# Optimization experiments

Hardware: AMD Instinct MI355X
Metric: run time of the kernel (lower is better)

## Reference

```python
import jax, jax.numpy as jnp
import numpy as np

F = 26          # number of sparse fields
V = 100000      # vocab per field
D = 32          # embedding dim
DENSE = 13
HID = (1024, 512, 256)
B = 16384


def setup_inputs() -> dict:
    key = jax.random.key(0)
    ks = jax.random.split(key, 16)
    x_sparse = jax.random.randint(ks[0], (B, F), 0, V, dtype=jnp.int32)
    x_dense = jax.random.normal(ks[1], (B, DENSE), dtype=jnp.float32)
    emb_tables = jax.random.normal(ks[2], (F, V, D), dtype=jnp.float32) * 0.05
    lin_tables = jax.random.normal(ks[3], (F, V), dtype=jnp.float32) * 0.05
    dnn_in = F * D + DENSE
    dims = (dnn_in,) + HID
    params = {}
    for i in range(len(HID)):
        params[f'W{i}'] = jax.random.normal(ks[4 + i], (dims[i], dims[i + 1]), dtype=jnp.float32) * (1.0 / np.sqrt(dims[i]))
        params[f'b{i}'] = jnp.zeros((dims[i + 1],), dtype=jnp.float32)
    Wout = jax.random.normal(ks[10], (HID[-1], 1), dtype=jnp.float32) * (1.0 / np.sqrt(HID[-1]))
    bout = jnp.zeros((1,), dtype=jnp.float32)
    return dict(x_sparse=x_sparse, x_dense=x_dense, emb_tables=emb_tables,
                lin_tables=lin_tables,
                W0=params['W0'], b0=params['b0'],
                W1=params['W1'], b1=params['b1'],
                W2=params['W2'], b2=params['b2'],
                Wout=Wout, bout=bout)


def reference(x_sparse, x_dense, emb_tables, lin_tables,
              W0, b0, W1, b1, W2, b2, Wout, bout):
    f_idx = jnp.arange(F)[None, :]            # [1, F]
    # batched multi-field gather: [B, F, D] and [B, F]
    emb = emb_tables[f_idx, x_sparse]          # [B, F, D]
    lin = lin_tables[f_idx, x_sparse]          # [B, F]
    linear_logit = lin.sum(axis=1)             # [B]
    # FM pairwise sum_{i<j} <e_i, e_j> via sum-square identity
    s = emb.sum(axis=1)                        # [B, D]
    fm_logit = 0.5 * ((s * s).sum(axis=-1) - (emb * emb).sum(axis=(1, 2)))  # [B]
    # DNN on concatenated embeddings + dense feats
    h = jnp.concatenate([emb.reshape(emb.shape[0], F * D), x_dense], axis=1)
    h = jax.nn.relu(h @ W0 + b0)
    h = jax.nn.relu(h @ W1 + b1)
    h = jax.nn.relu(h @ W2 + b2)
    dnn_logit = (h @ Wout + bout)[:, 0]        # [B]
    return jax.nn.sigmoid(linear_logit + fm_logit + dnn_logit)
```

## Files before the change

### kernel.cpp

```cpp
#include <hip/hip_runtime.h>
#include <math.h>


typedef __attribute__((ext_vector_type(8))) short shortx8;
typedef __attribute__((ext_vector_type(4))) float floatx4;

#define AS1 __attribute__((address_space(1)))
#define AS3 __attribute__((address_space(3)))

__device__ __forceinline__ void load_lds_16(const void* g, void* l) {
    __builtin_amdgcn_global_load_lds((AS1 void*)g, (AS3 void*)l, 16, 0, 0);
}

__device__ __forceinline__ unsigned short f2bf(float x) {
    union { float f; unsigned int u; } v; v.f = x;
    unsigned int r = v.u + 0x7fffu + ((v.u >> 16) & 1u);
    return (unsigned short)(r >> 16);
}

__global__ void wtrans(const float* __restrict__ W, unsigned short* __restrict__ Wt,
                       int K, int N, int Kpad)
{
    __shared__ float tile[32][33];
    const int k0 = blockIdx.x * 32, n0 = blockIdx.y * 32;
    const int tx = threadIdx.x, ty = threadIdx.y;
#pragma unroll
    for (int i = 0; i < 32; i += 8) {
        int k = k0 + ty + i;
        tile[ty + i][tx] = (k < K) ? W[(size_t)k * N + (n0 + tx)] : 0.f;
    }
    __syncthreads();
#pragma unroll
    for (int i = 0; i < 32; i += 8) {
        int n = n0 + ty + i, kk = k0 + tx;
        Wt[(size_t)n * Kpad + kk] = f2bf(tile[tx][ty + i]);
    }
}

__global__ __launch_bounds__(256)
void gather_fm(const int* __restrict__ xs, const float* __restrict__ xd,
               const float* __restrict__ emb, const float* __restrict__ lint,
               unsigned short* __restrict__ h0, float* __restrict__ lg)
{
    const int lane = threadIdx.x & 63;
    const int wave = threadIdx.x >> 6;
    const int b = blockIdx.x * 4 + wave;

    int idx = 0; float linv = 0.f;
    if (lane < 26) {
        idx = xs[b * 26 + lane];
        linv = lint[(size_t)lane * 100000 + idx];
    }
    const int d = lane & 31;
    const int half = lane >> 5;
    float s = 0.f, sq = 0.f;
    unsigned short* hrow = h0 + (size_t)b * 864;
#pragma unroll
    for (int it = 0; it < 13; ++it) {
        int f = it * 2 + half;
        int fidx = __shfl(idx, f);
        float v = emb[((size_t)f * 100000 + (size_t)fidx) * 32 + d];
        s += v; sq += v * v;
        hrow[f * 32 + d] = f2bf(v);
    }
    s += __shfl_xor(s, 32);
    float t = 0.25f * s * s - 0.5f * sq + linv;
#pragma unroll
    for (int off = 32; off >= 1; off >>= 1) t += __shfl_xor(t, off);
    if (lane == 0) lg[b] = t;

    if (lane < 13) {
        hrow[832 + lane] = f2bf(xd[b * 13 + lane]);
    } else if (lane < 32) {
        hrow[832 + lane] = 0;
    }
}

__global__ __launch_bounds__(256, 2)
void gemm_bign(const unsigned short* __restrict__ X,
               const unsigned short* __restrict__ Wt,
               const float* __restrict__ bias,
               unsigned short* __restrict__ Y,
               int M, int N, int K)
{
    __shared__ alignas(16) unsigned short As[128 * 32];
    __shared__ alignas(16) unsigned short Bs[256 * 32];

    const int tid  = threadIdx.x;
    const int lane = tid & 63;
    const int wave = tid >> 6;
    const int bm = blockIdx.x * 128;
    const int bn = blockIdx.y * 256;
    const int wm = (wave & 1) * 64;
    const int wn = (wave >> 1) * 128;
    const int lrow  = lane & 15;
    const int lquad = lane >> 4;

    floatx4 acc[4][8];
    const floatx4 z4 = {0.f, 0.f, 0.f, 0.f};
#pragma unroll
    for (int i = 0; i < 4; ++i)
#pragma unroll
        for (int j = 0; j < 8; ++j) acc[i][j] = z4;

    const int ar = tid >> 2, akp = (tid & 3) << 3;

    for (int k0 = 0; k0 < K; k0 += 32) {
        load_lds_16(X + (size_t)(bm + ar) * K + (k0 + akp), As + (size_t)tid * 8);
        load_lds_16(X + (size_t)(bm + ar + 64) * K + (k0 + akp), As + (size_t)(tid + 256) * 8);
#pragma unroll
        for (int q = 0; q < 4; ++q) {
            int c = tid + q * 256;
            load_lds_16(Wt + (size_t)(bn + (c >> 2)) * K + (k0 + akp), Bs + (size_t)c * 8);
        }
        __syncthreads();

        shortx8 a[4];
#pragma unroll
        for (int i = 0; i < 4; ++i)
            a[i] = *(const shortx8*)(As + (wm + i * 16 + lrow) * 32 + lquad * 8);
#pragma unroll
        for (int j = 0; j < 8; ++j) {
            shortx8 b = *(const shortx8*)(Bs + (wn + j * 16 + lrow) * 32 + lquad * 8);
#pragma unroll
            for (int i = 0; i < 4; ++i)
                acc[i][j] = __builtin_amdgcn_mfma_f32_16x16x32_bf16(a[i], b, acc[i][j], 0, 0, 0);
        }
        __syncthreads();
    }

#pragma unroll
    for (int i = 0; i < 4; ++i) {
        const int row = bm + wm + i * 16 + lquad * 4;
#pragma unroll
        for (int j = 0; j < 8; ++j) {
            const int col = bn + wn + j * 16 + lrow;
            const float bv = bias[col];
#pragma unroll
            for (int r = 0; r < 4; ++r) {
                float v = fmaxf(acc[i][j][r] + bv, 0.f);
                Y[(size_t)(row + r) * N + col] = f2bf(v);
            }
        }
    }
}

__global__ __launch_bounds__(256)
void gemm_bias_relu(const unsigned short* __restrict__ X,
                    const unsigned short* __restrict__ Wt,
                    const float* __restrict__ bias,
                    unsigned short* __restrict__ Y,
                    int M, int N, int K)
{
    __shared__ alignas(16) unsigned short As[128 * 32];
    __shared__ alignas(16) unsigned short Bs[128 * 32];

    const int tid  = threadIdx.x;
    const int lane = tid & 63;
    const int wave = tid >> 6;
    const int bm = blockIdx.x * 128;
    const int bn = blockIdx.y * 128;
    const int wm = (wave & 1) * 64;
    const int wn = (wave >> 1) * 64;
    const int lrow  = lane & 15;
    const int lquad = lane >> 4;

    floatx4 acc[4][4];
    const floatx4 z4 = {0.f, 0.f, 0.f, 0.f};
#pragma unroll
    for (int i = 0; i < 4; ++i)
#pragma unroll
        for (int j = 0; j < 4; ++j) acc[i][j] = z4;

    const int r0 = tid >> 2, kp0 = (tid & 3) << 3;

    for (int k0 = 0; k0 < K; k0 += 32) {
        load_lds_16(X  + (size_t)(bm + r0) * K + (k0 + kp0), As + (size_t)tid * 8);
        load_lds_16(Wt + (size_t)(bn + r0) * K + (k0 + kp0), Bs + (size_t)tid * 8);
        load_lds_16(X  + (size_t)(bm + r0 + 64) * K + (k0 + kp0), As + (size_t)(tid + 256) * 8);
        load_lds_16(Wt + (size_t)(bn + r0 + 64) * K + (k0 + kp0), Bs + (size_t)(tid + 256) * 8);
        __syncthreads();

        shortx8 a[4], b[4];
#pragma unroll
        for (int i = 0; i < 4; ++i)
            a[i] = *(const shortx8*)(As + (wm + i * 16 + lrow) * 32 + lquad * 8);
#pragma unroll
        for (int j = 0; j < 4; ++j)
            b[j] = *(const shortx8*)(Bs + (wn + j * 16 + lrow) * 32 + lquad * 8);
#pragma unroll
        for (int i = 0; i < 4; ++i)
#pragma unroll
            for (int j = 0; j < 4; ++j)
                acc[i][j] = __builtin_amdgcn_mfma_f32_16x16x32_bf16(a[i], b[j], acc[i][j], 0, 0, 0);
        __syncthreads();
    }

#pragma unroll
    for (int i = 0; i < 4; ++i) {
        const int row = bm + wm + i * 16 + lquad * 4;
#pragma unroll
        for (int j = 0; j < 4; ++j) {
            const int col = bn + wn + j * 16 + lrow;
            const float bv = bias[col];
#pragma unroll
            for (int r = 0; r < 4; ++r) {
                float v = fmaxf(acc[i][j][r] + bv, 0.f);
                Y[(size_t)(row + r) * N + col] = f2bf(v);
            }
        }
    }
}

__global__ __launch_bounds__(256)
void gemm3_final(const unsigned short* __restrict__ X,
                 const unsigned short* __restrict__ Wt,
                 const float* __restrict__ bias,
                 const float* __restrict__ Wo,
                 const float* __restrict__ bo,
                 const float* __restrict__ lg,
                 float* __restrict__ out)
{
    const int K = 512;
    __shared__ alignas(16) unsigned short As[64 * 32];
    __shared__ alignas(16) unsigned short Bs[256 * 32];
    __shared__ float red[4][64];

    const int tid  = threadIdx.x;
    const int lane = tid & 63;
    const int wave = tid >> 6;
    const int bm = blockIdx.x * 64;
    const int wn = wave * 64;
    const int lrow  = lane & 15;
    const int lquad = lane >> 4;

    floatx4 acc[4][4];
    const floatx4 z4 = {0.f, 0.f, 0.f, 0.f};
#pragma unroll
    for (int i = 0; i < 4; ++i)
#pragma unroll
        for (int j = 0; j < 4; ++j) acc[i][j] = z4;

    const int ar = tid >> 2, akp = (tid & 3) << 3;

    for (int k0 = 0; k0 < K; k0 += 32) {
        load_lds_16(X + (size_t)(bm + ar) * K + (k0 + akp), As + (size_t)tid * 8);
#pragma unroll
        for (int q = 0; q < 4; ++q) {
            int c = tid + q * 256;
            load_lds_16(Wt + (size_t)(c >> 2) * K + (k0 + akp), Bs + (size_t)c * 8);
        }
        __syncthreads();

        shortx8 a[4], b[4];
#pragma unroll
        for (int i = 0; i < 4; ++i)
            a[i] = *(const shortx8*)(As + (i * 16 + lrow) * 32 + lquad * 8);
#pragma unroll
        for (int j = 0; j < 4; ++j)
            b[j] = *(const shortx8*)(Bs + (wn + j * 16 + lrow) * 32 + lquad * 8);
#pragma unroll
        for (int i = 0; i < 4; ++i)
#pragma unroll
            for (int j = 0; j < 4; ++j)
                acc[i][j] = __builtin_amdgcn_mfma_f32_16x16x32_bf16(a[i], b[j], acc[i][j], 0, 0, 0);
        __syncthreads();
    }

    float bv[4], wv[4];
#pragma unroll
    for (int j = 0; j < 4; ++j) {
        int col = wn + j * 16 + lrow;
        bv[j] = bias[col];
        wv[j] = Wo[col];
    }
#pragma unroll
    for (int i = 0; i < 4; ++i) {
#pragma unroll
        for (int r = 0; r < 4; ++r) {
            float p = 0.f;
#pragma unroll
            for (int j = 0; j < 4; ++j) {
                float v = fmaxf(acc[i][j][r] + bv[j], 0.f);
                p += v * wv[j];
            }
            p += __shfl_xor(p, 1);
            p += __shfl_xor(p, 2);
            p += __shfl_xor(p, 4);
            p += __shfl_xor(p, 8);
            if (lrow == 0) red[wave][i * 16 + lquad * 4 + r] = p;
        }
    }
    __syncthreads();
    if (tid < 64) {
        float s = red[0][tid] + red[1][tid] + red[2][tid] + red[3][tid];
        float x = s + bo[0] + lg[bm + tid];
        out[bm + tid] = 1.f / (1.f + expf(-x));
    }
}

extern "C" void kernel_launch(void* const* d_in, const int* in_sizes, int n_in,
                              void* d_out, int out_size, void* d_ws, size_t ws_size,
                              hipStream_t stream)
{
    const int*   xs = (const int*)d_in[0];
    const float* xd = (const float*)d_in[1];
    const float* em = (const float*)d_in[2];
    const float* li = (const float*)d_in[3];
    const float* W0 = (const float*)d_in[4];
    const float* b0 = (const float*)d_in[5];
    const float* W1 = (const float*)d_in[6];
    const float* b1 = (const float*)d_in[7];
    const float* W2 = (const float*)d_in[8];
    const float* b2 = (const float*)d_in[9];
    const float* Wo = (const float*)d_in[10];
    const float* bo = (const float*)d_in[11];
    float* out = (float*)d_out;

    char* ws = (char*)d_ws;
    unsigned short* h0  = (unsigned short*)(ws);
    unsigned short* h1  = (unsigned short*)(ws + 28311552);
    unsigned short* h2  = (unsigned short*)(ws);
    unsigned short* Wt0 = (unsigned short*)(ws + 61865984);
    unsigned short* Wt1 = (unsigned short*)(ws + 63635456);
    unsigned short* Wt2 = (unsigned short*)(ws + 64684032);
    float*          lg  = (float*)(ws + 64946176);

    dim3 tb(32, 8);
    wtrans<<<dim3(27, 32), tb, 0, stream>>>(W0, Wt0, 845, 1024, 864);
    wtrans<<<dim3(32, 16), tb, 0, stream>>>(W1, Wt1, 1024, 512, 1024);
    wtrans<<<dim3(16, 8),  tb, 0, stream>>>(W2, Wt2, 512, 256, 512);

    gather_fm<<<4096, 256, 0, stream>>>(xs, xd, em, li, h0, lg);

    gemm_bign<<<dim3(128, 4), 256, 0, stream>>>(h0, Wt0, b0, h1, 16384, 1024, 864);
    gemm_bias_relu<<<dim3(128, 4), 256, 0, stream>>>(h1, Wt1, b1, h2, 16384, 512, 1024);
    gemm3_final<<<256, 256, 0, stream>>>(h2, Wt2, b2, Wo, bo, lg, out);
}
```

Baseline: 499.2 us.

## Fuse weight transposes into gather kernel, widen GEMM K-tile, reuse big-N GEMM

Merges the three weight transpose/convert launches into the gather+FM kernel by giving it extra blocks that each handle one transpose tile, removing launch overhead and letting the transposes overlap with the gather. Pads the first-layer K from 864 to 896 so the K loop can step by 64. Doubles the K tile of the large GEMM to 64 to halve barrier count per K, and drops the separate 128x128 GEMM in favour of the 128x256 kernel for layer 2. This uses twice the LDS per block, which may lower occupancy, and layer 2 now launches only 256 blocks.

```diff
diff --git a/kernel.cpp b/kernel.cpp
--- a/kernel.cpp
+++ b/kernel.cpp
@@ -18,12 +18,13 @@
     return (unsigned short)(r >> 16);
 }
 
-__global__ void wtrans(const float* __restrict__ W, unsigned short* __restrict__ Wt,
-                       int K, int N, int Kpad)
+__device__ __forceinline__
+void wtrans_tile(const float* __restrict__ W, unsigned short* __restrict__ Wt,
+                 int K, int N, int Kpad, int bx, int by, int tid)
 {
     __shared__ float tile[32][33];
-    const int k0 = blockIdx.x * 32, n0 = blockIdx.y * 32;
-    const int tx = threadIdx.x, ty = threadIdx.y;
+    const int k0 = bx * 32, n0 = by * 32;
+    const int tx = tid & 31, ty = tid >> 5;
 #pragma unroll
     for (int i = 0; i < 32; i += 8) {
         int k = k0 + ty + i;
@@ -38,13 +39,28 @@
 }
 
 __global__ __launch_bounds__(256)
-void gather_fm(const int* __restrict__ xs, const float* __restrict__ xd,
-               const float* __restrict__ emb, const float* __restrict__ lint,
-               unsigned short* __restrict__ h0, float* __restrict__ lg)
-{
-    const int lane = threadIdx.x & 63;
-    const int wave = threadIdx.x >> 6;
-    const int b = blockIdx.x * 4 + wave;
+void prep(const int* __restrict__ xs, const float* __restrict__ xd,
+          const float* __restrict__ emb, const float* __restrict__ lint,
+          const float* __restrict__ W0, const float* __restrict__ W1,
+          const float* __restrict__ W2,
+          unsigned short* __restrict__ h0, float* __restrict__ lg,
+          unsigned short* __restrict__ Wt0, unsigned short* __restrict__ Wt1,
+          unsigned short* __restrict__ Wt2)
+{
+    const int bid = blockIdx.x;
+    const int tid = threadIdx.x;
+
+    if (bid >= 4096) {
+        int t = bid - 4096;
+        if (t < 896)       wtrans_tile(W0, Wt0, 845, 1024, 896, t % 28, t / 28, tid);
+        else if (t < 1408) wtrans_tile(W1, Wt1, 1024, 512, 1024, (t - 896) % 32, (t - 896) / 32, tid);
+        else               wtrans_tile(W2, Wt2, 512, 256, 512, (t - 1408) % 16, (t - 1408) / 16, tid);
+        return;
+    }
+
+    const int lane = tid & 63;
+    const int wave = tid >> 6;
+    const int b = bid * 4 + wave;
 
     int idx = 0; float linv = 0.f;
     if (lane < 26) {
@@ -54,7 +70,7 @@
     const int d = lane & 31;
     const int half = lane >> 5;
     float s = 0.f, sq = 0.f;
-    unsigned short* hrow = h0 + (size_t)b * 864;
+    unsigned short* hrow = h0 + (size_t)b * 896;
 #pragma unroll
     for (int it = 0; it < 13; ++it) {
         int f = it * 2 + half;
@@ -69,11 +85,8 @@
     for (int off = 32; off >= 1; off >>= 1) t += __shfl_xor(t, off);
     if (lane == 0) lg[b] = t;
 
-    if (lane < 13) {
-        hrow[832 + lane] = f2bf(xd[b * 13 + lane]);
-    } else if (lane < 32) {
-        hrow[832 + lane] = 0;
-    }
+    if (lane < 13) hrow[832 + lane] = f2bf(xd[b * 13 + lane]);
+    else           hrow[832 + lane] = 0;
 }
 
 __global__ __launch_bounds__(256, 2)
@@ -83,8 +96,8 @@
                unsigned short* __restrict__ Y,
                int M, int N, int K)
 {
-    __shared__ alignas(16) unsigned short As[128 * 32];
-    __shared__ alignas(16) unsigned short Bs[256 * 32];
+    __shared__ alignas(16) unsigned short As[128 * 64];
+    __shared__ alignas(16) unsigned short Bs[256 * 64];
 
     const int tid  = threadIdx.x;
     const int lane = tid & 63;
@@ -103,28 +116,34 @@
 #pragma unroll
         for (int j = 0; j < 8; ++j) acc[i][j] = z4;
 
-    const int ar = tid >> 2, akp = (tid & 3) << 3;
-
-    for (int k0 = 0; k0 < K; k0 += 32) {
-        load_lds_16(X + (size_t)(bm + ar) * K + (k0 + akp), As + (size_t)tid * 8);
-        load_lds_16(X + (size_t)(bm + ar + 64) * K + (k0 + akp), As + (size_t)(tid + 256) * 8);
+    for (int k0 = 0; k0 < K; k0 += 64) {
 #pragma unroll
         for (int q = 0; q < 4; ++q) {
             int c = tid + q * 256;
-            load_lds_16(Wt + (size_t)(bn + (c >> 2)) * K + (k0 + akp), Bs + (size_t)c * 8);
-        }
-        __syncthreads();
-
-        shortx8 a[4];
-#pragma unroll
-        for (int i = 0; i < 4; ++i)
-            a[i] = *(const shortx8*)(As + (wm + i * 16 + lrow) * 32 + lquad * 8);
-#pragma unroll
-        for (int j = 0; j < 8; ++j) {
-            shortx8 b = *(const shortx8*)(Bs + (wn + j * 16 + lrow) * 32 + lquad * 8);
+            load_lds_16(X + (size_t)(bm + (c >> 3)) * K + (k0 + (c & 7) * 8),
+                        As + (size_t)c * 8);
+        }
+#pragma unroll
+        for (int q = 0; q < 8; ++q) {
+            int c = tid + q * 256;
+            load_lds_16(Wt + (size_t)(bn + (c >> 3)) * K + (k0 + (c & 7) * 8),
+                        Bs + (size_t)c * 8);
+        }
+        __syncthreads();
+
+#pragma unroll
+        for (int s = 0; s < 2; ++s) {
+            shortx8 a[4];
 #pragma unroll
             for (int i = 0; i < 4; ++i)
-                acc[i][j] = __builtin_amdgcn_mfma_f32_16x16x32_bf16(a[i], b, acc[i][j], 0, 0, 0);
+                a[i] = *(const shortx8*)(As + (wm + i * 16 + lrow) * 64 + s * 32 + lquad * 8);
+#pragma unroll
+            for (int j = 0; j < 8; ++j) {
+                shortx8 b = *(const shortx8*)(Bs + (wn + j * 16 + lrow) * 64 + s * 32 + lquad * 8);
+#pragma unroll
+                for (int i = 0; i < 4; ++i)
+                    acc[i][j] = __builtin_amdgcn_mfma_f32_16x16x32_bf16(a[i], b, acc[i][j], 0, 0, 0);
+            }
         }
         __syncthreads();
     }
@@ -134,73 +153,6 @@
         const int row = bm + wm + i * 16 + lquad * 4;
 #pragma unroll
         for (int j = 0; j < 8; ++j) {
-            const int col = bn + wn + j * 16 + lrow;
-            const float bv = bias[col];
-#pragma unroll
-            for (int r = 0; r < 4; ++r) {
-                float v = fmaxf(acc[i][j][r] + bv, 0.f);
-                Y[(size_t)(row + r) * N + col] = f2bf(v);
-            }
-        }
-    }
-}
-
-__global__ __launch_bounds__(256)
-void gemm_bias_relu(const unsigned short* __restrict__ X,
-                    const unsigned short* __restrict__ Wt,
-                    const float* __restrict__ bias,
-                    unsigned short* __restrict__ Y,
-                    int M, int N, int K)
-{
-    __shared__ alignas(16) unsigned short As[128 * 32];
-    __shared__ alignas(16) unsigned short Bs[128 * 32];
-
-    const int tid  = threadIdx.x;
-    const int lane = tid & 63;
-    const int wave = tid >> 6;
-    const int bm = blockIdx.x * 128;
-    const int bn = blockIdx.y * 128;
-    const int wm = (wave & 1) * 64;
-    const int wn = (wave >> 1) * 64;
-    const int lrow  = lane & 15;
-    const int lquad = lane >> 4;
-
-    floatx4 acc[4][4];
-    const floatx4 z4 = {0.f, 0.f, 0.f, 0.f};
-#pragma unroll
-    for (int i = 0; i < 4; ++i)
-#pragma unroll
-        for (int j = 0; j < 4; ++j) acc[i][j] = z4;
-
-    const int r0 = tid >> 2, kp0 = (tid & 3) << 3;
-
-    for (int k0 = 0; k0 < K; k0 += 32) {
-        load_lds_16(X  + (size_t)(bm + r0) * K + (k0 + kp0), As + (size_t)tid * 8);
-        load_lds_16(Wt + (size_t)(bn + r0) * K + (k0 + kp0), Bs + (size_t)tid * 8);
-        load_lds_16(X  + (size_t)(bm + r0 + 64) * K + (k0 + kp0), As + (size_t)(tid + 256) * 8);
-        load_lds_16(Wt + (size_t)(bn + r0 + 64) * K + (k0 + kp0), Bs + (size_t)(tid + 256) * 8);
-        __syncthreads();
-
-        shortx8 a[4], b[4];
-#pragma unroll
-        for (int i = 0; i < 4; ++i)
-            a[i] = *(const shortx8*)(As + (wm + i * 16 + lrow) * 32 + lquad * 8);
-#pragma unroll
-        for (int j = 0; j < 4; ++j)
-            b[j] = *(const shortx8*)(Bs + (wn + j * 16 + lrow) * 32 + lquad * 8);
-#pragma unroll
-        for (int i = 0; i < 4; ++i)
-#pragma unroll
-            for (int j = 0; j < 4; ++j)
-                acc[i][j] = __builtin_amdgcn_mfma_f32_16x16x32_bf16(a[i], b[j], acc[i][j], 0, 0, 0);
-        __syncthreads();
-    }
-
-#pragma unroll
-    for (int i = 0; i < 4; ++i) {
-        const int row = bm + wm + i * 16 + lquad * 4;
-#pragma unroll
-        for (int j = 0; j < 4; ++j) {
             const int col = bn + wn + j * 16 + lrow;
             const float bv = bias[col];
 #pragma unroll
@@ -319,21 +271,16 @@
 
     char* ws = (char*)d_ws;
     unsigned short* h0  = (unsigned short*)(ws);
-    unsigned short* h1  = (unsigned short*)(ws + 28311552);
+    unsigned short* h1  = (unsigned short*)(ws + 29360128);
     unsigned short* h2  = (unsigned short*)(ws);
-    unsigned short* Wt0 = (unsigned short*)(ws + 61865984);
-    unsigned short* Wt1 = (unsigned short*)(ws + 63635456);
-    unsigned short* Wt2 = (unsigned short*)(ws + 64684032);
-    float*          lg  = (float*)(ws + 64946176);
-
-    dim3 tb(32, 8);
-    wtrans<<<dim3(27, 32), tb, 0, stream>>>(W0, Wt0, 845, 1024, 864);
-    wtrans<<<dim3(32, 16), tb, 0, stream>>>(W1, Wt1, 1024, 512, 1024);
-    wtrans<<<dim3(16, 8),  tb, 0, stream>>>(W2, Wt2, 512, 256, 512);
-
-    gather_fm<<<4096, 256, 0, stream>>>(xs, xd, em, li, h0, lg);
-
-    gemm_bign<<<dim3(128, 4), 256, 0, stream>>>(h0, Wt0, b0, h1, 16384, 1024, 864);
-    gemm_bias_relu<<<dim3(128, 4), 256, 0, stream>>>(h1, Wt1, b1, h2, 16384, 512, 1024);
+    unsigned short* Wt0 = (unsigned short*)(ws + 62914560);
+    unsigned short* Wt1 = (unsigned short*)(ws + 64749568);
+    unsigned short* Wt2 = (unsigned short*)(ws + 65798144);
+    float*          lg  = (float*)(ws + 66060288);
+
+    prep<<<5632, 256, 0, stream>>>(xs, xd, em, li, W0, W1, W2, h0, lg, Wt0, Wt1, Wt2);
+
+    gemm_bign<<<dim3(128, 4), 256, 0, stream>>>(h0, Wt0, b0, h1, 16384, 1024, 896);
+    gemm_bign<<<dim3(128, 2), 256, 0, stream>>>(h1, Wt1, b1, h2, 16384, 512, 1024);
     gemm3_final<<<256, 256, 0, stream>>>(h2, Wt2, b2, Wo, bo, lg, out);
 }
```

New measurement: 493.5 us. No clear change (-1.1%).
